# Optimization experiments

Hardware: AMD Instinct MI355X
Metric: run time of the kernel (lower is better)

Reference implementation:

```python
import jax, jax.numpy as jnp
import numpy as np

T, B, D, A, L = 256, 256, 512, 32, 3
EPS = 1e-6

def _layernorm(x, scale, bias):
    mu = jnp.mean(x, axis=-1, keepdims=True)
    var = jnp.mean(jnp.square(x - mu), axis=-1, keepdims=True)
    return (x - mu) * jax.lax.rsqrt(var + EPS) * scale + bias

def setup_inputs() -> dict:
    key = jax.random.key(0)
    ks = jax.random.split(key, 16)
    def orth(k, shape, scale):
        a = jax.random.normal(k, shape, dtype=jnp.float32)
        q, r = jnp.linalg.qr(a)
        q = q * jnp.sign(jnp.diagonal(r))
        return (scale * q).astype(jnp.float32)
    inp = {
        'hidden': jnp.zeros((B, D), jnp.float32),
        'obs': jax.random.normal(ks[0], (T, B, D), jnp.float32),
        'dones': jax.random.randint(ks[1], (T, B), 0, 2) > 0,
        'avail_actions': jax.random.randint(ks[2], (T, B, A), 0, 2).astype(jnp.int32),
        # MLP stack: 3 Dense(D) + LayerNorm
        'Wm': jnp.stack([orth(jax.random.fold_in(ks[3], l), (D, D), np.sqrt(2)) for l in range(L)]),
        'bm': jnp.zeros((L, D), jnp.float32),
        'lns': jnp.ones((L, D), jnp.float32),
        'lnb': jnp.zeros((L, D), jnp.float32),
        # GRUCell params: input denses ir/iz/in (with bias), hidden denses hr/hz (no bias), hn (bias)
        'Wi': jnp.stack([jax.random.normal(jax.random.fold_in(ks[4], g), (D, D), jnp.float32) / np.sqrt(D) for g in range(3)]),
        'bi': jnp.zeros((3, D), jnp.float32),
        'Wh': jnp.stack([orth(jax.random.fold_in(ks[5], g), (D, D), 1.0) for g in range(3)]),
        'bhn': jnp.zeros((D,), jnp.float32),
        # actor head
        'Wo': orth(ks[6], (D, D), 2.0),
        'bo': jnp.zeros((D,), jnp.float32),
        'ln2s': jnp.ones((D,), jnp.float32),
        'ln2b': jnp.zeros((D,), jnp.float32),
        'Wa': orth(ks[7], (D, A), 0.01),
        'ba': jnp.zeros((A,), jnp.float32),
    }
    return inp

def reference(hidden, obs, dones, avail_actions, Wm, bm, lns, lnb, Wi, bi, Wh, bhn, Wo, bo, ln2s, ln2b, Wa, ba):
    # MLP encoder: Dense -> LayerNorm -> ReLU, x num_layers
    e = obs  # [T,B,D]
    for l in range(Wm.shape[0]):
        e = jax.nn.relu(_layernorm(e @ Wm[l] + bm[l], lns[l], lnb[l]))
    # time-scanned GRU with reset-masked carry (reset -> zeros carry)
    def step(h, xs):
        x, d = xs  # x:[B,D], d:[B]
        h = jnp.where(d[:, None], jnp.zeros_like(h), h)
        r = jax.nn.sigmoid(x @ Wi[0] + bi[0] + h @ Wh[0])
        z = jax.nn.sigmoid(x @ Wi[1] + bi[1] + h @ Wh[1])
        n = jnp.tanh(x @ Wi[2] + bi[2] + r * (h @ Wh[2] + bhn))
        h_new = (1.0 - z) * n + z * h
        return h_new, h_new
    hidden, y = jax.lax.scan(step, hidden, (e, dones))  # y:[T,B,D]
    # actor head
    am = jax.nn.relu(_layernorm(y @ Wo + bo, ln2s, ln2b))
    logits = am @ Wa + ba
    unavail = 1.0 - avail_actions.astype(logits.dtype)
    action_logits = logits - unavail * 1e10
    return hidden, action_logits
```

## Files before the change

kernel.cpp:

```cpp
#include <hip/hip_runtime.h>
#include <hip/hip_bf16.h>
#include <math.h>


#define TTT 256
#define BBB 256
#define DDD 512
#define ACT 32
#define MMM (TTT*BBB)

typedef short bf16x8 __attribute__((ext_vector_type(8)));
typedef float f32x4 __attribute__((ext_vector_type(4)));
typedef unsigned short u16;

__device__ inline u16 f2bf(float f) {
    unsigned int u = __float_as_uint(f);
    u += 0x7fffu + ((u >> 16) & 1u);
    return (u16)(u >> 16);
}
__device__ inline float bf2f(u16 h) { return __uint_as_float(((unsigned int)h) << 16); }

#define AL_RLX(p)  __hip_atomic_load((p), __ATOMIC_RELAXED, __HIP_MEMORY_SCOPE_AGENT)

__global__ __launch_bounds__(256) void transpose_cvt_k(
    const float* __restrict__ in, u16* __restrict__ out, int ostride)
{
    __shared__ float tile[32][33];
    const int c = threadIdx.x & 31;
    const int r0 = threadIdx.x >> 5;
    const int bx = blockIdx.x, by = blockIdx.y;
#pragma unroll
    for (int p = 0; p < 4; p++) {
        int r = r0 + p * 8;
        tile[r][c] = in[(size_t)(by * 32 + r) * DDD + bx * 32 + c];
    }
    __syncthreads();
#pragma unroll
    for (int p = 0; p < 4; p++) {
        int r = r0 + p * 8;
        out[(size_t)(bx * 32 + r) * ostride + by * 32 + c] = f2bf(tile[c][r]);
    }
}

template<bool AF32>
__global__ __launch_bounds__(256) void gemm_bf16_k(
    const void* __restrict__ Aptr, const u16* __restrict__ Bt,
    const float* __restrict__ bias, u16* __restrict__ C, int N)
{
    __shared__ u16 As[128 * 64];
    __shared__ u16 Bs[128 * 64];
    const int tid = threadIdx.x;
    const int row0 = blockIdx.x * 128;
    const int col0 = blockIdx.y * 128;
    const int lane = tid & 63, wid = tid >> 6;
    const int wr = wid >> 1, wc = wid & 1;
    const int lm = lane & 15, lq = lane >> 4;

    f32x4 acc[4][4];
#pragma unroll
    for (int i = 0; i < 4; i++)
#pragma unroll
        for (int j = 0; j < 4; j++) acc[i][j] = (f32x4){0.f, 0.f, 0.f, 0.f};

    for (int kc = 0; kc < 8; kc++) {
        const int k0 = kc * 64;
#pragma unroll
        for (int p = 0; p < 4; p++) {
            int g = p * 256 + tid;
            int row = g >> 3, j = g & 7;
            bf16x8 v;
            if (AF32) {
                const float* s = (const float*)Aptr + (size_t)(row0 + row) * DDD + k0 + j * 8;
                float4 a0 = *(const float4*)s;
                float4 a1 = *(const float4*)(s + 4);
                v[0] = (short)f2bf(a0.x); v[1] = (short)f2bf(a0.y);
                v[2] = (short)f2bf(a0.z); v[3] = (short)f2bf(a0.w);
                v[4] = (short)f2bf(a1.x); v[5] = (short)f2bf(a1.y);
                v[6] = (short)f2bf(a1.z); v[7] = (short)f2bf(a1.w);
            } else {
                v = *(const bf16x8*)((const u16*)Aptr + (size_t)(row0 + row) * DDD + k0 + j * 8);
            }
            *(bf16x8*)(As + row * 64 + ((j ^ (row & 7)) << 3)) = v;
        }
#pragma unroll
        for (int p = 0; p < 4; p++) {
            int g = p * 256 + tid;
            int n = g >> 3, j = g & 7;
            bf16x8 v = *(const bf16x8*)(Bt + (size_t)(col0 + n) * DDD + k0 + j * 8);
            *(bf16x8*)(Bs + n * 64 + ((j ^ (n & 7)) << 3)) = v;
        }
        __syncthreads();
#pragma unroll
        for (int ks = 0; ks < 2; ks++) {
            bf16x8 af[4], bfr[4];
#pragma unroll
            for (int i = 0; i < 4; i++) {
                int row = wr * 64 + i * 16 + lm;
                af[i] = *(const bf16x8*)(As + row * 64 + (((ks * 4 + lq) ^ (row & 7)) << 3));
            }
#pragma unroll
            for (int j = 0; j < 4; j++) {
                int n = wc * 64 + j * 16 + lm;
                bfr[j] = *(const bf16x8*)(Bs + n * 64 + (((ks * 4 + lq) ^ (n & 7)) << 3));
            }
#pragma unroll
            for (int i = 0; i < 4; i++)
#pragma unroll
                for (int j = 0; j < 4; j++)
                    acc[i][j] = __builtin_amdgcn_mfma_f32_16x16x32_bf16(af[i], bfr[j], acc[i][j], 0, 0, 0);
        }
        __syncthreads();
    }
#pragma unroll
    for (int j = 0; j < 4; j++) {
        int col = col0 + wc * 64 + j * 16 + lm;
        float bj = bias[col];
#pragma unroll
        for (int i = 0; i < 4; i++) {
            int rb = row0 + wr * 64 + i * 16 + lq * 4;
#pragma unroll
            for (int r = 0; r < 4; r++)
                C[(size_t)(rb + r) * N + col] = f2bf(acc[i][j][r] + bj);
        }
    }
}

__global__ __launch_bounds__(256) void ln_relu_k(
    u16* __restrict__ X, const float* __restrict__ gamma, const float* __restrict__ beta)
{
    const int tid = threadIdx.x;
    const int lane = tid & 63;
    const size_t row = (size_t)blockIdx.x * 4 + (tid >> 6);
    const int c0 = lane * 8;
    u16* px = X + row * DDD + c0;
    bf16x8 v = *(const bf16x8*)px;
    float f[8]; float s = 0.f, s2 = 0.f;
#pragma unroll
    for (int i = 0; i < 8; i++) { f[i] = bf2f((u16)v[i]); s += f[i]; s2 += f[i] * f[i]; }
#pragma unroll
    for (int off = 32; off; off >>= 1) { s += __shfl_xor(s, off); s2 += __shfl_xor(s2, off); }
    float mu = s * (1.f / (float)DDD);
    float rs = rsqrtf(s2 * (1.f / (float)DDD) - mu * mu + 1e-6f);
    float4 g0 = *(const float4*)(gamma + c0), g1 = *(const float4*)(gamma + c0 + 4);
    float4 b0 = *(const float4*)(beta + c0),  b1 = *(const float4*)(beta + c0 + 4);
    float gg[8] = {g0.x, g0.y, g0.z, g0.w, g1.x, g1.y, g1.z, g1.w};
    float bb[8] = {b0.x, b0.y, b0.z, b0.w, b1.x, b1.y, b1.z, b1.w};
    bf16x8 o;
#pragma unroll
    for (int i = 0; i < 8; i++) {
        float yv = (f[i] - mu) * rs * gg[i] + bb[i];
        o[i] = (short)f2bf(fmaxf(yv, 0.f));
    }
    *(bf16x8*)px = o;
}

__global__ __launch_bounds__(256) void logits_k(
    const u16* __restrict__ AM, const float* __restrict__ Wa,
    const float* __restrict__ ba, const int* __restrict__ avail,
    float* __restrict__ out)
{
    __shared__ float xs[8][DDD];
    const int tid = threadIdx.x;
    const size_t row0 = (size_t)blockIdx.x * 8;
    for (int g = tid; g < 8 * 64; g += 256) {
        int r = g >> 6, c8 = (g & 63) * 8;
        bf16x8 v = *(const bf16x8*)(AM + (row0 + r) * DDD + c8);
#pragma unroll
        for (int i = 0; i < 8; i++) xs[r][c8 + i] = bf2f((u16)v[i]);
    }
    __syncthreads();
    const int r = tid >> 5, a = tid & 31;
    float acc = 0.f;
    for (int k = 0; k < DDD; k += 4) {
        float4 xv = *(const float4*)&xs[r][k];
        acc = fmaf(xv.x, Wa[(k + 0) * ACT + a], acc);
        acc = fmaf(xv.y, Wa[(k + 1) * ACT + a], acc);
        acc = fmaf(xv.z, Wa[(k + 2) * ACT + a], acc);
        acc = fmaf(xv.w, Wa[(k + 3) * ACT + a], acc);
    }
    size_t o = (row0 + r) * ACT + a;
    float v = acc + ba[a];
    if (avail[o] == 0) v -= 1e10f;
    out[o] = v;
}

__global__ __launch_bounds__(256) void depth_build_k(
    const int* __restrict__ dones,
    int* __restrict__ keyA, int* __restrict__ pidxA,
    int* __restrict__ counts, int* __restrict__ maxk)
{
    __shared__ int lc[8 * 512];
    __shared__ int lmax[8];
    const int b = threadIdx.x;
    const int e = b >> 5;
    for (int i = b; i < 8 * 512; i += 256) lc[i] = 0;
    if (b < 8) lmax[b] = 0;
    __syncthreads();
    int dprev = 0, mx = 0;
    for (int t = 0; t < TTT; t++) {
        int pos = t * BBB + b;
        int d, pi, k;
        if (dones[pos] != 0)       { d = 0; pi = -1;       k = 0; }
        else if (t == 0)           { d = 0; pi = -2 - b;   k = 1; }
        else                       { d = dprev + 1; pi = pos - BBB; k = d + 1; }
        keyA[pos] = k; pidxA[pos] = pi;
        atomicAdd(&lc[e * 512 + k], 1);
        mx = max(mx, k);
        dprev = d;
    }
    atomicMax(&lmax[e], mx);
    __syncthreads();
    for (int i = b; i < 8 * 512; i += 256) counts[i] = lc[i];
    if (b < 8) maxk[b] = lmax[b];
}

__global__ void scan_k(const int* __restrict__ counts, int* __restrict__ offs)
{
    int e = threadIdx.x;
    if (e < 8) {
        int s = 0;
        for (int i = 0; i < 512; i++) { offs[e * 512 + i] = s; s += counts[e * 512 + i]; }
    }
}

__global__ __launch_bounds__(256) void scatter_k(
    const int* __restrict__ keyA, const int* __restrict__ offs,
    int* __restrict__ cursor, int* __restrict__ list)
{
    __shared__ int lcnt[8 * 512];
    __shared__ int lbase[8 * 512];
    const int tid = threadIdx.x;
    for (int i = tid; i < 8 * 512; i += 256) lcnt[i] = 0;
    __syncthreads();
    int pos = blockIdx.x * 256 + tid;
    int b = pos & 255;
    int e = b >> 5;
    int k = keyA[pos];
    int rank = atomicAdd(&lcnt[e * 512 + k], 1);
    __syncthreads();
    for (int q = tid; q < 8 * 512; q += 256) {
        int c = lcnt[q];
        lbase[q] = c ? atomicAdd(&cursor[q], c) : 0;
    }
    __syncthreads();
    list[e * 8192 + offs[e * 512 + k] + lbase[e * 512 + k] + rank] = pos;
}

template<bool YF32>
__device__ __forceinline__ void gru_job(
    const u16* __restrict__ E, const float* __restrict__ hidden,
    const u16* __restrict__ Wstk, const float* __restrict__ bi,
    const float* __restrict__ bhn,
    const int* __restrict__ list, const int* __restrict__ pidxA,
    void* __restrict__ Yv,
    int off, int nd, int rt, int panel,
    u16* As, int* posL, int* pidxL, int* sAnyH)
{
    const int tid = threadIdx.x;
    const int w = tid >> 6, lane = tid & 63;
    const int lm = lane & 15, lq = lane >> 4;

    bool hasH = false;
    if (tid < 64) {
        int idx = rt * 64 + tid;
        int p = (idx < nd) ? list[off + idx] : -1;
        int pi = (p >= 0) ? pidxA[p] : -1;
        posL[tid] = p;
        pidxL[tid] = pi;
        hasH = (p >= 0) && (pi != -1);
        unsigned long long m = __ballot(hasH);
        if (tid == 0) *sAnyH = (m != 0ULL);
    }
    __syncthreads();
    const bool skipH = !(*sAnyH);

    f32x4 a01[4][4], aX[4][2], aH[4][2];
#pragma unroll
    for (int mt = 0; mt < 4; mt++) {
#pragma unroll
        for (int q = 0; q < 4; q++) a01[mt][q] = (f32x4){0.f, 0.f, 0.f, 0.f};
#pragma unroll
        for (int q = 0; q < 2; q++) {
            aX[mt][q] = (f32x4){0.f, 0.f, 0.f, 0.f};
            aH[mt][q] = (f32x4){0.f, 0.f, 0.f, 0.f};
        }
    }

    const int cb = panel * 128 + w * 32;
    const u16* wp[6];
#pragma unroll
    for (int ct = 0; ct < 6; ct++) {
        int gate = ct >> 1;
        int nglob = gate * 512 + cb + ((ct & 1) << 4) + lm;
        wp[ct] = Wstk + (size_t)nglob * 1024 + lq * 8;
    }

    const int nkc = skipH ? 2 : 4;
    for (int kc = 0; kc < nkc; kc++) {
#pragma unroll
        for (int it = 0; it < 8; it++) {
            int g = it * 256 + tid;
            int row = g >> 5, jg = g & 31;
            int kglob = kc * 256 + jg * 8;
            bf16x8 v = (bf16x8){0, 0, 0, 0, 0, 0, 0, 0};
            int p = posL[row];
            if (p >= 0) {
                if (kglob < 512) {
                    v = *(const bf16x8*)(E + (size_t)p * DDD + kglob);
                } else {
                    int k2 = kglob - 512;
                    int pi = pidxL[row];
                    if (pi >= 0) {
                        if (YF32) {
                            const float* s = (const float*)Yv + (size_t)pi * DDD + k2;
                            float4 a0 = *(const float4*)s;
                            float4 a1 = *(const float4*)(s + 4);
                            v[0] = (short)f2bf(a0.x); v[1] = (short)f2bf(a0.y);
                            v[2] = (short)f2bf(a0.z); v[3] = (short)f2bf(a0.w);
                            v[4] = (short)f2bf(a1.x); v[5] = (short)f2bf(a1.y);
                            v[6] = (short)f2bf(a1.z); v[7] = (short)f2bf(a1.w);
                        } else {
                            v = *(const bf16x8*)((const u16*)Yv + (size_t)pi * DDD + k2);
                        }
                    } else if (pi <= -2) {
                        const float* s = hidden + (size_t)(-pi - 2) * DDD + k2;
                        float4 a0 = *(const float4*)s;
                        float4 a1 = *(const float4*)(s + 4);
                        v[0] = (short)f2bf(a0.x); v[1] = (short)f2bf(a0.y);
                        v[2] = (short)f2bf(a0.z); v[3] = (short)f2bf(a0.w);
                        v[4] = (short)f2bf(a1.x); v[5] = (short)f2bf(a1.y);
                        v[6] = (short)f2bf(a1.z); v[7] = (short)f2bf(a1.w);
                    }
                }
            }
            *(bf16x8*)(As + row * 256 + ((jg ^ (row & 31)) << 3)) = v;
        }
        __syncthreads();

        const bool xpart = (kc < 2);
        const int kgb = kc * 256;
        bf16x8 bfA[6], bfB[6];

#define LOADW(B, KG) \
    _Pragma("unroll") \
    for (int ct = 0; ct < 6; ct++) B[ct] = *(const bf16x8*)(wp[ct] + (KG));

#define COMPW(B, S) \
    _Pragma("unroll") \
    for (int mt = 0; mt < 4; mt++) { \
        int row = mt * 16 + lm; \
        int jgr = (S) * 4 + lq; \
        bf16x8 af = *(const bf16x8*)(As + row * 256 + ((jgr ^ (row & 31)) << 3)); \
        a01[mt][0] = __builtin_amdgcn_mfma_f32_16x16x32_bf16(af, B[0], a01[mt][0], 0, 0, 0); \
        a01[mt][1] = __builtin_amdgcn_mfma_f32_16x16x32_bf16(af, B[1], a01[mt][1], 0, 0, 0); \
        a01[mt][2] = __builtin_amdgcn_mfma_f32_16x16x32_bf16(af, B[2], a01[mt][2], 0, 0, 0); \
        a01[mt][3] = __builtin_amdgcn_mfma_f32_16x16x32_bf16(af, B[3], a01[mt][3], 0, 0, 0); \
        if (xpart) { \
            aX[mt][0] = __builtin_amdgcn_mfma_f32_16x16x32_bf16(af, B[4], aX[mt][0], 0, 0, 0); \
            aX[mt][1] = __builtin_amdgcn_mfma_f32_16x16x32_bf16(af, B[5], aX[mt][1], 0, 0, 0); \
        } else { \
            aH[mt][0] = __builtin_amdgcn_mfma_f32_16x16x32_bf16(af, B[4], aH[mt][0], 0, 0, 0); \
            aH[mt][1] = __builtin_amdgcn_mfma_f32_16x16x32_bf16(af, B[5], aH[mt][1], 0, 0, 0); \
        } \
    }

        LOADW(bfA, kgb + 0 * 32);
#pragma unroll
        for (int sp = 0; sp < 4; sp++) {
            const int s0 = sp * 2, s1 = sp * 2 + 1;
            LOADW(bfB, kgb + s1 * 32);
            COMPW(bfA, s0);
            if (sp < 3) { LOADW(bfA, kgb + (s1 + 1) * 32); }
            COMPW(bfB, s1);
        }
#undef LOADW
#undef COMPW
        __syncthreads();
    }

#pragma unroll
    for (int mt = 0; mt < 4; mt++) {
#pragma unroll
        for (int r = 0; r < 4; r++) {
            int row = mt * 16 + lq * 4 + r;
            int p = posL[row];
            if (p < 0) continue;
            int pi = pidxL[row];
#pragma unroll
            for (int ct = 0; ct < 2; ct++) {
                int cglob = cb + ct * 16 + lm;
                float rpre = a01[mt][ct][r]     + bi[cglob];
                float zpre = a01[mt][2 + ct][r] + bi[512 + cglob];
                float xn   = aX[mt][ct][r]      + bi[1024 + cglob];
                float hn   = aH[mt][ct][r]      + bhn[cglob];
                float rg = 1.f / (1.f + __expf(-rpre));
                float zg = 1.f / (1.f + __expf(-zpre));
                float targ = xn + rg * hn;
                float t2 = __expf(-2.f * fabsf(targ));
                float ng = copysignf((1.f - t2) / (1.f + t2), targ);
                float hp = 0.f;
                if (pi >= 0)
                    hp = YF32 ? ((const float*)Yv)[(size_t)pi * DDD + cglob]
                              : bf2f(((const u16*)Yv)[(size_t)pi * DDD + cglob]);
                else if (pi <= -2)
                    hp = hidden[(size_t)(-pi - 2) * DDD + cglob];
                float hnew = (1.f - zg) * ng + zg * hp;
                if (YF32) ((float*)Yv)[(size_t)p * DDD + cglob] = hnew;
                else      ((u16*)Yv)[(size_t)p * DDD + cglob] = f2bf(hnew);
            }
        }
    }
    __syncthreads();
}

template<bool YF32>
__global__ __launch_bounds__(256, 2) void gru_depth_k(
    const u16* __restrict__ E, const float* __restrict__ hidden,
    const u16* __restrict__ Wstk, const float* __restrict__ bi,
    const float* __restrict__ bhn,
    const int* __restrict__ list, const int* __restrict__ offs,
    const int* __restrict__ counts, const int* __restrict__ maxk,
    const int* __restrict__ pidxA,
    void* __restrict__ Yv, float* __restrict__ hid_out,
    int* __restrict__ xcdCnt)
{
    __shared__ u16 As[64 * 256];
    __shared__ int posL[64], pidxL[64];
    __shared__ int sAnyH;
    const int tid = threadIdx.x;
    const int nblk = gridDim.x;
    const int e   = blockIdx.x & 7;
    const int xb  = blockIdx.x >> 3;
    const int nxb = nblk >> 3;

    const int MKe = maxk[e];
    const int* cnt_e = counts + e * 512;
    const int* off_e = offs + e * 512;
    const int lb = e * 8192;
    int* cnt = xcdCnt + e * 32;
    int round = 0;

    for (int k = 0; k <= MKe; k++) {
        const int nd = cnt_e[k];
        const int off = lb + off_e[k];
        const int njobs = ((nd + 63) >> 6) << 2;
        for (int lj = xb; lj < njobs; lj += nxb) {
            gru_job<YF32>(E, hidden, Wstk, bi, bhn, list, pidxA, Yv,
                          off, nd, lj >> 2, lj & 3, As, posL, pidxL, &sAnyH);
        }
        ++round;
        __syncthreads();
        if (tid == 0) {
            __hip_atomic_fetch_add(cnt, 1, __ATOMIC_RELAXED, __HIP_MEMORY_SCOPE_AGENT);
            const int target = round * nxb;
            while (AL_RLX(cnt) < target) __builtin_amdgcn_s_sleep(1);
        }
        __syncthreads();
    }

    for (int i = xb * 256 + tid; i < 32 * DDD; i += nxb * 256) {
        int b = 32 * e + (i >> 9), c = i & 511;
        size_t yi = (size_t)(65280 + b) * DDD + c;
        hid_out[(size_t)b * DDD + c] =
            YF32 ? ((const float*)Yv)[yi] : bf2f(((const u16*)Yv)[yi]);
    }
}

extern "C" void kernel_launch(void* const* d_in, const int* in_sizes, int n_in,
                              void* d_out, int out_size, void* d_ws, size_t ws_size,
                              hipStream_t stream)
{
    const float* hidden = (const float*)d_in[0];
    const float* obs    = (const float*)d_in[1];
    const int*   dones  = (const int*)d_in[2];
    const int*   avail  = (const int*)d_in[3];
    const float* Wm     = (const float*)d_in[4];
    const float* bm     = (const float*)d_in[5];
    const float* lns    = (const float*)d_in[6];
    const float* lnb    = (const float*)d_in[7];
    const float* Wi     = (const float*)d_in[8];
    const float* bi     = (const float*)d_in[9];
    const float* Wh     = (const float*)d_in[10];
    const float* bhn    = (const float*)d_in[11];
    const float* Wo     = (const float*)d_in[12];
    const float* bo     = (const float*)d_in[13];
    const float* ln2s   = (const float*)d_in[14];
    const float* ln2b   = (const float*)d_in[15];
    const float* Wa     = (const float*)d_in[16];
    const float* ba     = (const float*)d_in[17];
    float* out = (float*)d_out;

    char* w = (char*)d_ws;
    u16* Wstk = (u16*)w;  w += (size_t)1536 * 1024 * 2;
    u16* WmT  = (u16*)w;  w += (size_t)3 * DDD * DDD * 2;
    u16* WoT  = (u16*)w;  w += (size_t)DDD * DDD * 2;
    int* meta = (int*)w;  w += 65536;
    int* counts = meta;
    int* offs   = meta + 4096;
    int* cursor = meta + 8192;
    int* maxk   = meta + 12288;
    int* xcdCnt = meta + 12544;
    int* keyA   = (int*)w;  w += (size_t)MMM * 4;
    int* pidxA  = (int*)w;  w += (size_t)MMM * 4;
    int* list   = (int*)w;  w += (size_t)MMM * 4;
    u16* P = (u16*)w;       w += (size_t)MMM * DDD * 2;
    void* Yv = (void*)w;
    const size_t base = (size_t)(w - (char*)d_ws);
    const bool yf32 = (ws_size >= base + (size_t)MMM * DDD * 4);

    dim3 tgrid(16, 16);
    for (int l = 0; l < 3; l++)
        transpose_cvt_k<<<tgrid, 256, 0, stream>>>(Wm + (size_t)l * DDD * DDD, WmT + (size_t)l * DDD * DDD, DDD);
    transpose_cvt_k<<<tgrid, 256, 0, stream>>>(Wo, WoT, DDD);
    for (int g = 0; g < 3; g++) {
        transpose_cvt_k<<<tgrid, 256, 0, stream>>>(Wi + (size_t)g * DDD * DDD, Wstk + (size_t)g * 512 * 1024, 1024);
        transpose_cvt_k<<<tgrid, 256, 0, stream>>>(Wh + (size_t)g * DDD * DDD, Wstk + (size_t)g * 512 * 1024 + 512, 1024);
    }
    hipMemsetAsync(meta, 0, 65536, stream);

    depth_build_k<<<1, 256, 0, stream>>>(dones, keyA, pidxA, counts, maxk);
    scan_k<<<1, 64, 0, stream>>>(counts, offs);
    scatter_k<<<MMM / 256, 256, 0, stream>>>(keyA, offs, cursor, list);

    u16* Yq = (u16*)Yv;
    gemm_bf16_k<true><<<dim3(MMM / 128, 4), 256, 0, stream>>>(obs, WmT, bm, P, DDD);
    ln_relu_k<<<dim3(MMM / 4), 256, 0, stream>>>(P, lns, lnb);
    gemm_bf16_k<false><<<dim3(MMM / 128, 4), 256, 0, stream>>>(P, WmT + (size_t)DDD * DDD, bm + DDD, Yq, DDD);
    ln_relu_k<<<dim3(MMM / 4), 256, 0, stream>>>(Yq, lns + DDD, lnb + DDD);
    gemm_bf16_k<false><<<dim3(MMM / 128, 4), 256, 0, stream>>>(Yq, WmT + (size_t)2 * DDD * DDD, bm + 2 * DDD, P, DDD);
    ln_relu_k<<<dim3(MMM / 4), 256, 0, stream>>>(P, lns + 2 * DDD, lnb + 2 * DDD);

    {
        const void* fptr = yf32 ? (const void*)gru_depth_k<true>
                                : (const void*)gru_depth_k<false>;
        int occ = 0;
        hipError_t err = hipOccupancyMaxActiveBlocksPerMultiprocessor(&occ, fptr, 256, 0);
        if (err != hipSuccess || occ < 1) occ = 2;
        if (occ > 4) occ = 4;
        dim3 grid(occ * 256);
        if (yf32)
            gru_depth_k<true><<<grid, 256, 0, stream>>>(
                P, hidden, Wstk, bi, bhn, list, offs, counts, maxk, pidxA,
                Yv, out, xcdCnt);
        else
            gru_depth_k<false><<<grid, 256, 0, stream>>>(
                P, hidden, Wstk, bi, bhn, list, offs, counts, maxk, pidxA,
                Yv, out, xcdCnt);
    }

    if (yf32)
        gemm_bf16_k<true><<<dim3(MMM / 128, 4), 256, 0, stream>>>(Yv, WoT, bo, P, DDD);
    else
        gemm_bf16_k<false><<<dim3(MMM / 128, 4), 256, 0, stream>>>(Yv, WoT, bo, P, DDD);
    ln_relu_k<<<dim3(MMM / 4), 256, 0, stream>>>(P, ln2s, ln2b);
    logits_k<<<dim3(MMM / 8), 256, 0, stream>>>(P, Wa, ba, avail, out + BBB * DDD);
}
```

Before: 1.881 ms.

## Restrict GRU wave barriers to participating blocks and merge first two levels

New measurement: 1.922 ms. 2.2% more time.

```diff
diff --git a/kernel.cpp b/kernel.cpp
--- a/kernel.cpp
+++ b/kernel.cpp
@@ -20,7 +20,9 @@
 }
 __device__ inline float bf2f(u16 h) { return __uint_as_float(((unsigned int)h) << 16); }
 
-#define AL_RLX(p)  __hip_atomic_load((p), __ATOMIC_RELAXED, __HIP_MEMORY_SCOPE_AGENT)
+__device__ inline int rmw_read(int* p) {
+    return __hip_atomic_fetch_add(p, 0, __ATOMIC_RELAXED, __HIP_MEMORY_SCOPE_AGENT);
+}
 
 __global__ __launch_bounds__(256) void transpose_cvt_k(
     const float* __restrict__ in, u16* __restrict__ out, int ostride)
@@ -438,31 +440,63 @@
     const int* off_e = offs + e * 512;
     const int lb = e * 8192;
     int* cnt = xcdCnt + e * 32;
-    int round = 0;
-
-    for (int k = 0; k <= MKe; k++) {
+    int T = 0;
+
+    {
+        const int nd0 = cnt_e[0], nd1 = cnt_e[1];
+        const int nj0 = nd0 ? (((nd0 + 63) >> 6) << 2) : 0;
+        const int nj1 = nd1 ? (((nd1 + 63) >> 6) << 2) : 0;
+        const int njobs = nj0 + nj1;
+        const int p = (njobs < nxb) ? njobs : nxb;
+        if (p > 0 && xb < p) {
+            for (int lj = xb; lj < njobs; lj += p) {
+                if (lj < nj0)
+                    gru_job<YF32>(E, hidden, Wstk, bi, bhn, list, pidxA, Yv,
+                                  lb + off_e[0], nd0, lj >> 2, lj & 3,
+                                  As, posL, pidxL, &sAnyH);
+                else {
+                    int j1 = lj - nj0;
+                    gru_job<YF32>(E, hidden, Wstk, bi, bhn, list, pidxA, Yv,
+                                  lb + off_e[1], nd1, j1 >> 2, j1 & 3,
+                                  As, posL, pidxL, &sAnyH);
+                }
+            }
+            if (tid == 0)
+                __hip_atomic_fetch_add(cnt, 1, __ATOMIC_RELAXED, __HIP_MEMORY_SCOPE_AGENT);
+        }
+        T = p;
+    }
+
+    for (int k = 2; k <= MKe; k++) {
         const int nd = cnt_e[k];
-        const int off = lb + off_e[k];
-        const int njobs = ((nd + 63) >> 6) << 2;
-        for (int lj = xb; lj < njobs; lj += nxb) {
-            gru_job<YF32>(E, hidden, Wstk, bi, bhn, list, pidxA, Yv,
-                          off, nd, lj >> 2, lj & 3, As, posL, pidxL, &sAnyH);
-        }
-        ++round;
+        const int njobs = nd ? (((nd + 63) >> 6) << 2) : 0;
+        const int p = (njobs < nxb) ? njobs : nxb;
+        if (p > 0 && xb < p) {
+            if (tid == 0) {
+                while (rmw_read(cnt) < T) __builtin_amdgcn_s_sleep(2);
+            }
+            __syncthreads();
+            for (int lj = xb; lj < njobs; lj += p)
+                gru_job<YF32>(E, hidden, Wstk, bi, bhn, list, pidxA, Yv,
+                              lb + off_e[k], nd, lj >> 2, lj & 3,
+                              As, posL, pidxL, &sAnyH);
+            if (tid == 0)
+                __hip_atomic_fetch_add(cnt, 1, __ATOMIC_RELAXED, __HIP_MEMORY_SCOPE_AGENT);
+        }
+        T += p;
+    }
+
+    if (xb < 8) {
+        if (tid == 0) {
+            while (rmw_read(cnt) < T) __builtin_amdgcn_s_sleep(2);
+        }
         __syncthreads();
-        if (tid == 0) {
-            __hip_atomic_fetch_add(cnt, 1, __ATOMIC_RELAXED, __HIP_MEMORY_SCOPE_AGENT);
-            const int target = round * nxb;
-            while (AL_RLX(cnt) < target) __builtin_amdgcn_s_sleep(1);
-        }
-        __syncthreads();
-    }
-
-    for (int i = xb * 256 + tid; i < 32 * DDD; i += nxb * 256) {
-        int b = 32 * e + (i >> 9), c = i & 511;
-        size_t yi = (size_t)(65280 + b) * DDD + c;
-        hid_out[(size_t)b * DDD + c] =
-            YF32 ? ((const float*)Yv)[yi] : bf2f(((const u16*)Yv)[yi]);
+        for (int i = xb * 256 + tid; i < 32 * DDD; i += 8 * 256) {
+            int b = 32 * e + (i >> 9), c = i & 511;
+            size_t yi = (size_t)(65280 + b) * DDD + c;
+            hid_out[(size_t)b * DDD + c] =
+                YF32 ? ((const float*)Yv)[yi] : bf2f(((const u16*)Yv)[yi]);
+        }
     }
 }
 
```
